# Optimization experiments

Measured on AMD Instinct MI355X. Metric: run time of the kernel, lower is better.

## Reference

```python
import jax, jax.numpy as jnp
import numpy as np
import math

EPS_LN = 1e-5
SCALE = 16.0  # cosine_sim_scale


def layer_norm(x, g):
    mean = jnp.mean(x, axis=-1, keepdims=True)
    var = jnp.var(x, axis=-1, keepdims=True)  # biased, matches unbiased=False
    return (x - mean) * jax.lax.rsqrt(var + EPS_LN) * g


def l2norm(t):
    n = jnp.linalg.norm(t, axis=-1, keepdims=True)
    return t / jnp.maximum(n, 1e-12)


def setup_inputs() -> dict:
    key = jax.random.key(0)
    ks = jax.random.split(key, 4)
    b, n, dim, h, dh = 4, 2048, 1024, 8, 64
    inner = h * dh
    x = jax.random.normal(ks[0], (b, n, dim), dtype=jnp.float32)
    Wq = jax.random.normal(ks[1], (dim, inner), dtype=jnp.float32) * (dim ** -0.5)
    Wkv = jax.random.normal(ks[2], (dim, 2 * dh), dtype=jnp.float32) * (dim ** -0.5)
    Wout = jax.random.normal(ks[3], (inner, dim), dtype=jnp.float32) * (inner ** -0.5)
    norm_g = jnp.ones((dim,), dtype=jnp.float32)
    out_norm_g = jnp.ones((dim,), dtype=jnp.float32)
    return {"x": x, "norm_g": norm_g, "Wq": Wq, "Wkv": Wkv, "Wout": Wout,
            "out_norm_g": out_norm_g}


def reference(x, norm_g, Wq, Wkv, Wout, out_norm_g):
    b, n, dim = x.shape
    h = 8
    dh = Wkv.shape[-1] // 2
    xn = layer_norm(x, norm_g)
    q = xn @ Wq                      # [b, n, h*dh]
    kv = xn @ Wkv                    # [b, n, 2*dh]
    k, v = kv[..., :dh], kv[..., dh:]
    q = q.reshape(b, n, h, dh).transpose(0, 2, 1, 3)  # [b, h, n, dh]
    q = q * SCALE                    # cancelled by l2norm, kept for fidelity
    q = l2norm(q)
    k = l2norm(k)
    rs = math.sqrt(SCALE)
    q = q * rs
    k = k * rs
    sim = jnp.einsum('bhid,bjd->bhij', q, k)          # [b, h, n, n]
    attn = jax.nn.softmax(sim.astype(jnp.float32), axis=-1).astype(sim.dtype)
    out = jnp.einsum('bhij,bjd->bhid', attn, v)       # [b, h, n, dh]
    out = out.transpose(0, 2, 1, 3).reshape(b, n, h * dh)
    out = out @ Wout
    return layer_norm(out, out_norm_g)
```

## Files before the change

kernel.cpp:

```cpp
#include <hip/hip_runtime.h>
#include <hip/hip_bf16.h>

typedef __attribute__((ext_vector_type(8))) short short8;
typedef __attribute__((ext_vector_type(4))) float floatx4;
typedef __attribute__((ext_vector_type(16))) float floatx16;

__device__ __forceinline__ float bf2f(ushort u) {
    return __uint_as_float(((unsigned int)u) << 16);
}
__device__ __forceinline__ ushort f2bf(float f) {
    unsigned int u = __float_as_uint(f);
    unsigned int r = (u + 0x7FFFu + ((u >> 16) & 1u)) >> 16;
    return (ushort)r;
}
__device__ __forceinline__ unsigned int pk2(float a, float b) {
    union { __hip_bfloat162 h; unsigned int u; } cv;
    cv.h = __float22bfloat162_rn(make_float2(a, b));
    return cv.u;
}
__device__ __forceinline__ float scrub(float v, float lim) {
    return fminf(fmaxf(v, -lim), lim);
}
__device__ __forceinline__ void glds16(const ushort* g, ushort* l) {
    __builtin_amdgcn_global_load_lds((const __attribute__((address_space(1))) void*)g,
                                     (__attribute__((address_space(3))) void*)l, 16, 0, 0);
}

__device__ __forceinline__ bool detect_bf16(const ushort* __restrict__ probe) {
    const int lane = threadIdx.x & 63;
    ushort u = probe[(lane & 31) * 2];
    int e = (u >> 7) & 0xFF;
    bool pl = (e >= 117) && (e <= 131) && (lane < 32);
    return __popcll(__ballot(pl)) >= 16;
}

__device__ __forceinline__ void do_transpose(const void* __restrict__ in,
                                             ushort* __restrict__ out,
                                             int bx, int by, int in_rs, int out_rs,
                                             bool ib, ushort* tile ) {
    const int tx = threadIdx.x & 31, ty = threadIdx.x >> 5;
    #pragma unroll
    for (int rr = 0; rr < 32; rr += 8) {
        size_t idx = (size_t)(by * 32 + ty + rr) * in_rs + bx * 32 + tx;
        float v = ib ? bf2f(((const ushort*)in)[idx]) : ((const float*)in)[idx];
        tile[(ty + rr) * 33 + tx] = f2bf(scrub(v, 1e8f));
    }
    __syncthreads();
    #pragma unroll
    for (int rr = 0; rr < 32; rr += 8) {
        int r = bx * 32 + ty + rr;
        int c = by * 32 + tx;
        out[(size_t)r * out_rs + c] = tile[tx * 33 + (ty + rr)];
    }
}

__global__ __launch_bounds__(256) void prep_kernel(const void* __restrict__ xin,
                                                   const void* __restrict__ gin,
                                                   const void* __restrict__ Wq,
                                                   const void* __restrict__ Wkv,
                                                   ushort* __restrict__ xn,
                                                   ushort* __restrict__ wcatT,
                                                   const ushort* __restrict__ probe) {
    const bool ib = detect_bf16(probe);
    const int id = blockIdx.x;
    __shared__ ushort tile[32 * 33];
    __shared__ float red[8];

    if (id >= 8192) {
        if (id < 8704) {
            int t = id - 8192;
            do_transpose(Wq, wcatT, t & 15, t >> 4, 512, 1024, ib, tile);
        } else {
            int t = id - 8704;
            do_transpose(Wkv, wcatT + (size_t)512 * 1024, t & 3, t >> 2, 128, 1024, ib, tile);
        }
        return;
    }

    const int row = id;
    const int tid = threadIdx.x;
    float v0, v1, v2, v3, g0, g1, g2, g3;
    if (ib) {
        uint2 u = *(const uint2*)((const ushort*)xin + (size_t)row * 1024 + tid * 4);
        v0 = bf2f((ushort)(u.x & 0xFFFF)); v1 = bf2f((ushort)(u.x >> 16));
        v2 = bf2f((ushort)(u.y & 0xFFFF)); v3 = bf2f((ushort)(u.y >> 16));
        uint2 gu = *(const uint2*)((const ushort*)gin + tid * 4);
        g0 = bf2f((ushort)(gu.x & 0xFFFF)); g1 = bf2f((ushort)(gu.x >> 16));
        g2 = bf2f((ushort)(gu.y & 0xFFFF)); g3 = bf2f((ushort)(gu.y >> 16));
    } else {
        float4 xv = *(const float4*)((const float*)xin + (size_t)row * 1024 + tid * 4);
        v0 = xv.x; v1 = xv.y; v2 = xv.z; v3 = xv.w;
        float4 gv = *(const float4*)((const float*)gin + tid * 4);
        g0 = gv.x; g1 = gv.y; g2 = gv.z; g3 = gv.w;
    }
    v0 = scrub(v0, 1e8f); v1 = scrub(v1, 1e8f); v2 = scrub(v2, 1e8f); v3 = scrub(v3, 1e8f);
    g0 = scrub(g0, 1e8f); g1 = scrub(g1, 1e8f); g2 = scrub(g2, 1e8f); g3 = scrub(g3, 1e8f);

    float s  = v0 + v1 + v2 + v3;
    float sq = v0 * v0 + v1 * v1 + v2 * v2 + v3 * v3;
    #pragma unroll
    for (int off = 1; off < 64; off <<= 1) {
        s  += __shfl_xor(s, off);
        sq += __shfl_xor(sq, off);
    }
    const int w = tid >> 6, lane = tid & 63;
    if (lane == 0) { red[w] = s; red[w + 4] = sq; }
    __syncthreads();
    float S  = red[0] + red[1] + red[2] + red[3];
    float SQ = red[4] + red[5] + red[6] + red[7];

    float mean = S * (1.0f / 1024.0f);
    float var  = SQ * (1.0f / 1024.0f) - mean * mean;
    float rstd = rsqrtf(fmaxf(var, 0.0f) + 1e-5f);

    uint2 ov;
    ov.x = pk2((v0 - mean) * rstd * g0, (v1 - mean) * rstd * g1);
    ov.y = pk2((v2 - mean) * rstd * g2, (v3 - mean) * rstd * g3);
    *(uint2*)(xn + (size_t)row * 1024 + tid * 4) = ov;
}

__global__ __launch_bounds__(256) void wout_tr_kernel(const void* __restrict__ Wout,
                                                      ushort* __restrict__ woT,
                                                      const ushort* __restrict__ probe) {
    const bool ib = detect_bf16(probe);
    __shared__ ushort tile[32 * 33];
    do_transpose(Wout, woT, blockIdx.x, blockIdx.y, 1024, 512, ib, tile);
}

__global__ __launch_bounds__(256) void ln2_kernel(const ushort* __restrict__ y,
                                                  const void* __restrict__ gin,
                                                  void* __restrict__ out,
                                                  const ushort* __restrict__ probe) {
    const bool ob = detect_bf16(probe);
    const int row = blockIdx.x;
    const int tid = threadIdx.x;

    uint2 u = *(const uint2*)(y + (size_t)row * 1024 + tid * 4);
    float v0 = scrub(bf2f((ushort)(u.x & 0xFFFF)), 1e8f);
    float v1 = scrub(bf2f((ushort)(u.x >> 16)),    1e8f);
    float v2 = scrub(bf2f((ushort)(u.y & 0xFFFF)), 1e8f);
    float v3 = scrub(bf2f((ushort)(u.y >> 16)),    1e8f);

    float g0, g1, g2, g3;
    if (ob) {
        uint2 gu = *(const uint2*)((const ushort*)gin + tid * 4);
        g0 = bf2f((ushort)(gu.x & 0xFFFF)); g1 = bf2f((ushort)(gu.x >> 16));
        g2 = bf2f((ushort)(gu.y & 0xFFFF)); g3 = bf2f((ushort)(gu.y >> 16));
    } else {
        float4 gv = *(const float4*)((const float*)gin + tid * 4);
        g0 = gv.x; g1 = gv.y; g2 = gv.z; g3 = gv.w;
    }
    g0 = scrub(g0, 1e8f); g1 = scrub(g1, 1e8f); g2 = scrub(g2, 1e8f); g3 = scrub(g3, 1e8f);

    float s  = v0 + v1 + v2 + v3;
    float sq = v0 * v0 + v1 * v1 + v2 * v2 + v3 * v3;
    #pragma unroll
    for (int off = 1; off < 64; off <<= 1) {
        s  += __shfl_xor(s, off);
        sq += __shfl_xor(sq, off);
    }
    __shared__ float red[8];
    const int w = tid >> 6, lane = tid & 63;
    if (lane == 0) { red[w] = s; red[w + 4] = sq; }
    __syncthreads();
    float S  = red[0] + red[1] + red[2] + red[3];
    float SQ = red[4] + red[5] + red[6] + red[7];

    float mean = S * (1.0f / 1024.0f);
    float var  = SQ * (1.0f / 1024.0f) - mean * mean;
    float rstd = rsqrtf(fmaxf(var, 0.0f) + 1e-5f);

    float o0 = (v0 - mean) * rstd * g0;
    float o1 = (v1 - mean) * rstd * g1;
    float o2 = (v2 - mean) * rstd * g2;
    float o3 = (v3 - mean) * rstd * g3;
    if (ob) {
        uint2 ov;
        ov.x = pk2(o0, o1);
        ov.y = pk2(o2, o3);
        *(uint2*)((ushort*)out + (size_t)row * 1024 + tid * 4) = ov;
    } else {
        *(float4*)((float*)out + (size_t)row * 1024 + tid * 4) = make_float4(o0, o1, o2, o3);
    }
}

__global__ __launch_bounds__(256) void gemm_qkv(const ushort* __restrict__ A,
                                                const ushort* __restrict__ Bt,
                                                ushort* __restrict__ qb,
                                                ushort* __restrict__ kb,
                                                ushort* __restrict__ vt) {
    __shared__ ushort a_t[64 * 32];
    __shared__ ushort b_t[64 * 32];

    const int bx = blockIdx.x;
    const int n0 = bx * 64, m0 = blockIdx.y * 64;
    const int tid = threadIdx.x;
    const int w = tid >> 6, lane = tid & 63;
    const int fm = lane & 15, quad = lane >> 4;
    const int K = 1024;

    const ushort* ag = A + (size_t)(m0 + (tid >> 2)) * K + (tid & 3) * 8;
    const ushort* bg = Bt + (size_t)(n0 + (tid >> 2)) * K + (tid & 3) * 8;
    ushort* la = a_t + w * 512;
    ushort* lb = b_t + w * 512;

    floatx4 acc[4];
    floatx4 zero4 = {0.0f, 0.0f, 0.0f, 0.0f};
    #pragma unroll
    for (int nt = 0; nt < 4; nt++) acc[nt] = zero4;

    union U8 { uint4 u4; short8 s8; };

    for (int k0 = 0; k0 < K; k0 += 32) {
        __syncthreads();
        glds16(ag + k0, la);
        glds16(bg + k0, lb);
        __syncthreads();

        U8 af;
        af.u4 = *(const uint4*)&a_t[(w * 16 + fm) * 32 + quad * 8];
        #pragma unroll
        for (int nt = 0; nt < 4; nt++) {
            U8 bf;
            bf.u4 = *(const uint4*)&b_t[(nt * 16 + fm) * 32 + quad * 8];
            acc[nt] = __builtin_amdgcn_mfma_f32_16x16x32_bf16(af.s8, bf.s8, acc[nt], 0, 0, 0);
        }
    }

    if (bx < 9) {
        const float qsc = (bx < 8) ? 5.7707801636f : 4.0f;
        float sc[4];
        #pragma unroll
        for (int r = 0; r < 4; r++) {
            float ss = acc[0][r] * acc[0][r] + acc[1][r] * acc[1][r]
                     + acc[2][r] * acc[2][r] + acc[3][r] * acc[3][r];
            ss += __shfl_xor(ss, 1);
            ss += __shfl_xor(ss, 2);
            ss += __shfl_xor(ss, 4);
            ss += __shfl_xor(ss, 8);
            sc[r] = qsc / fmaxf(sqrtf(ss), 1e-12f);
        }
        ushort* op;
        int rs;
        if (bx < 8) { op = qb + n0; rs = 512; }
        else        { op = kb;      rs = 64;  }
        #pragma unroll
        for (int nt = 0; nt < 4; nt++)
            #pragma unroll
            for (int r = 0; r < 4; r++)
                op[(size_t)(m0 + w * 16 + quad * 4 + r) * rs + nt * 16 + fm] =
                    f2bf(acc[nt][r] * sc[r]);
    } else {
        const int b = m0 >> 11;
        const int jb = (m0 & 2047) + w * 16 + quad * 4;
        ushort* vb = vt + (size_t)b * 64 * 2048 + jb;
        #pragma unroll
        for (int nt = 0; nt < 4; nt++) {
            uint2 pv;
            pv.x = pk2(acc[nt][0], acc[nt][1]);
            pv.y = pk2(acc[nt][2], acc[nt][3]);
            *(uint2*)(vb + (size_t)(nt * 16 + fm) * 2048) = pv;
        }
    }
}

__global__ __launch_bounds__(256) void gemm_bt128(const ushort* __restrict__ A,
                                                  const ushort* __restrict__ Bt,
                                                  ushort* __restrict__ C,
                                                  int M, int N, int K) {
    __shared__ ushort a_t[128][32];
    __shared__ ushort b_t[128][32];

    const int n0 = blockIdx.x * 128, m0 = blockIdx.y * 128;
    const int tid = threadIdx.x;
    const int w = tid >> 6, lane = tid & 63;
    const int fm = lane & 15, quad = lane >> 4;

    const int c0 = tid, c1 = tid + 256;
    const ushort* ag0 = A + (size_t)(m0 + (c0 >> 2)) * K + (c0 & 3) * 8;
    const ushort* ag1 = A + (size_t)(m0 + (c1 >> 2)) * K + (c1 & 3) * 8;
    const ushort* bg0 = Bt + (size_t)(n0 + (c0 >> 2)) * K + (c0 & 3) * 8;
    const ushort* bg1 = Bt + (size_t)(n0 + (c1 >> 2)) * K + (c1 & 3) * 8;
    ushort* la0 = &a_t[0][0] + w * 512;
    ushort* la1 = &a_t[0][0] + 2048 + w * 512;
    ushort* lb0 = &b_t[0][0] + w * 512;
    ushort* lb1 = &b_t[0][0] + 2048 + w * 512;

    floatx4 acc[2][8];
    floatx4 zero4 = {0.0f, 0.0f, 0.0f, 0.0f};
    #pragma unroll
    for (int mt = 0; mt < 2; mt++)
        #pragma unroll
        for (int nt = 0; nt < 8; nt++) acc[mt][nt] = zero4;

    union U8 { uint4 u4; short8 s8; };

    for (int k0 = 0; k0 < K; k0 += 32) {
        __syncthreads();
        glds16(ag0 + k0, la0);
        glds16(ag1 + k0, la1);
        glds16(bg0 + k0, lb0);
        glds16(bg1 + k0, lb1);
        __syncthreads();

        U8 af[2];
        #pragma unroll
        for (int mt = 0; mt < 2; mt++)
            af[mt].u4 = *(const uint4*)&a_t[w * 32 + mt * 16 + fm][quad * 8];
        #pragma unroll
        for (int nt = 0; nt < 8; nt++) {
            U8 bf;
            bf.u4 = *(const uint4*)&b_t[nt * 16 + fm][quad * 8];
            acc[0][nt] = __builtin_amdgcn_mfma_f32_16x16x32_bf16(af[0].s8, bf.s8, acc[0][nt], 0, 0, 0);
            acc[1][nt] = __builtin_amdgcn_mfma_f32_16x16x32_bf16(af[1].s8, bf.s8, acc[1][nt], 0, 0, 0);
        }
    }

    #pragma unroll
    for (int mt = 0; mt < 2; mt++)
        #pragma unroll
        for (int nt = 0; nt < 8; nt++)
            #pragma unroll
            for (int r = 0; r < 4; r++)
                C[(size_t)(m0 + w * 32 + mt * 16 + quad * 4 + r) * N + n0 + nt * 16 + fm] =
                    f2bf(acc[mt][nt][r]);
}

__global__ __launch_bounds__(512, 4) void attn_kernel(const ushort* __restrict__ q,
                                                      const ushort* __restrict__ kb,
                                                      const ushort* __restrict__ vt,
                                                      ushort* __restrict__ out) {
    __shared__ ushort k_t[2][2][64 * 64];
    __shared__ ushort v_t[2][2][64 * 64];

    const int i0 = blockIdx.x * 128;
    const int h0 = blockIdx.y, b = blockIdx.z;
    const int tid = threadIdx.x, w = tid >> 6, lane = tid & 63;
    const int qg = w & 3;
    const int kh = w >> 2;
    const int cq = lane & 31;
    const int hi = lane >> 5;
    const int sw = cq & 7;

    union U8 { uint4 u4; short8 s8; };

    const ushort* qbase = q + (size_t)(b * 2048 + i0 + qg * 32 + cq) * 512 + h0 * 64 + hi * 8;
    U8 qf[4];
    #pragma unroll
    for (int dm = 0; dm < 4; dm++) qf[dm].u4 = *(const uint4*)(qbase + dm * 16);

    floatx16 acc0, acc1;
    #pragma unroll
    for (int i = 0; i < 16; i++) { acc0[i] = 0.0f; acc1[i] = 0.0f; }
    float lsum = 0.0f;

    const ushort* kbb = kb + (size_t)b * 2048 * 64;
    const ushort* vtb = vt + (size_t)b * 64 * 2048;

    const int srow = w * 8 + (lane >> 3);
    const int soct = (lane & 7) ^ (srow & 7);
    const int prow = (srow & ~12) | ((srow & 4) << 1) | ((srow & 8) >> 1);
    const ushort* kgl = kbb + (size_t)prow * 64 + soct * 8;
    const ushort* vgl = vtb + (size_t)srow * 2048 + soct * 8;
    ushort* kldb = &k_t[0][0][0] + w * 512;
    ushort* vldb = &v_t[0][0][0] + w * 512;

    int koff[4];
    #pragma unroll
    for (int i = 0; i < 4; i++) koff[i] = ((2 * i + hi) ^ sw) * 8;
    const int rb0 = cq * 64, rb1 = rb0 + 2048;

    auto compute = [&](const ushort* ktile, const ushort* vtile) {
        U8 pb0, pb1, pb2, pb3;
        {
            floatx16 st;
            #pragma unroll
            for (int i = 0; i < 16; i++) st[i] = -23.0831206f;
            #pragma unroll
            for (int dm = 0; dm < 4; dm++) {
                U8 kf;
                kf.u4 = *(const uint4*)&ktile[rb0 + koff[dm]];
                st = __builtin_amdgcn_mfma_f32_32x32x16_bf16(kf.s8, qf[dm].s8, st, 0, 0, 0);
            }
            float p_[16];
            #pragma unroll
            for (int r = 0; r < 16; r++) p_[r] = exp2f(st[r]);
            lsum += (((p_[0] + p_[1]) + (p_[2] + p_[3])) + ((p_[4] + p_[5]) + (p_[6] + p_[7])))
                  + (((p_[8] + p_[9]) + (p_[10] + p_[11])) + ((p_[12] + p_[13]) + (p_[14] + p_[15])));
            pb0.u4.x = pk2(p_[0], p_[1]);   pb0.u4.y = pk2(p_[2], p_[3]);
            pb0.u4.z = pk2(p_[4], p_[5]);   pb0.u4.w = pk2(p_[6], p_[7]);
            pb1.u4.x = pk2(p_[8], p_[9]);   pb1.u4.y = pk2(p_[10], p_[11]);
            pb1.u4.z = pk2(p_[12], p_[13]); pb1.u4.w = pk2(p_[14], p_[15]);
        }
        {
            floatx16 st;
            #pragma unroll
            for (int i = 0; i < 16; i++) st[i] = -23.0831206f;
            #pragma unroll
            for (int dm = 0; dm < 4; dm++) {
                U8 kf;
                kf.u4 = *(const uint4*)&ktile[rb1 + koff[dm]];
                st = __builtin_amdgcn_mfma_f32_32x32x16_bf16(kf.s8, qf[dm].s8, st, 0, 0, 0);
            }
            float p_[16];
            #pragma unroll
            for (int r = 0; r < 16; r++) p_[r] = exp2f(st[r]);
            lsum += (((p_[0] + p_[1]) + (p_[2] + p_[3])) + ((p_[4] + p_[5]) + (p_[6] + p_[7])))
                  + (((p_[8] + p_[9]) + (p_[10] + p_[11])) + ((p_[12] + p_[13]) + (p_[14] + p_[15])));
            pb2.u4.x = pk2(p_[0], p_[1]);   pb2.u4.y = pk2(p_[2], p_[3]);
            pb2.u4.z = pk2(p_[4], p_[5]);   pb2.u4.w = pk2(p_[6], p_[7]);
            pb3.u4.x = pk2(p_[8], p_[9]);   pb3.u4.y = pk2(p_[10], p_[11]);
            pb3.u4.z = pk2(p_[12], p_[13]); pb3.u4.w = pk2(p_[14], p_[15]);
        }
        U8 vf;
        vf.u4 = *(const uint4*)&vtile[rb0 + koff[0]];
        acc0 = __builtin_amdgcn_mfma_f32_32x32x16_bf16(vf.s8, pb0.s8, acc0, 0, 0, 0);
        vf.u4 = *(const uint4*)&vtile[rb0 + koff[1]];
        acc0 = __builtin_amdgcn_mfma_f32_32x32x16_bf16(vf.s8, pb1.s8, acc0, 0, 0, 0);
        vf.u4 = *(const uint4*)&vtile[rb0 + koff[2]];
        acc0 = __builtin_amdgcn_mfma_f32_32x32x16_bf16(vf.s8, pb2.s8, acc0, 0, 0, 0);
        vf.u4 = *(const uint4*)&vtile[rb0 + koff[3]];
        acc0 = __builtin_amdgcn_mfma_f32_32x32x16_bf16(vf.s8, pb3.s8, acc0, 0, 0, 0);
        vf.u4 = *(const uint4*)&vtile[rb1 + koff[0]];
        acc1 = __builtin_amdgcn_mfma_f32_32x32x16_bf16(vf.s8, pb0.s8, acc1, 0, 0, 0);
        vf.u4 = *(const uint4*)&vtile[rb1 + koff[1]];
        acc1 = __builtin_amdgcn_mfma_f32_32x32x16_bf16(vf.s8, pb1.s8, acc1, 0, 0, 0);
        vf.u4 = *(const uint4*)&vtile[rb1 + koff[2]];
        acc1 = __builtin_amdgcn_mfma_f32_32x32x16_bf16(vf.s8, pb2.s8, acc1, 0, 0, 0);
        vf.u4 = *(const uint4*)&vtile[rb1 + koff[3]];
        acc1 = __builtin_amdgcn_mfma_f32_32x32x16_bf16(vf.s8, pb3.s8, acc1, 0, 0, 0);
    };

    glds16(kgl, kldb);
    glds16(kgl + (size_t)1024 * 64, kldb + 4096);
    glds16(vgl, vldb);
    glds16(vgl + 1024, vldb + 4096);
    __syncthreads();

    const ushort* mk = &k_t[0][0][0] + kh * 4096;
    const ushort* mv = &v_t[0][0][0] + kh * 4096;

    for (int s = 0; s < 16; s++) {
        const int cur = (s & 1) << 13;
        const int nxt = cur ^ 8192;
        if (s < 15) {
            const int j = (s + 1) * 64;
            glds16(kgl + (size_t)j * 64, kldb + nxt);
            glds16(kgl + (size_t)(1024 + j) * 64, kldb + nxt + 4096);
            glds16(vgl + j, vldb + nxt);
            glds16(vgl + 1024 + j, vldb + nxt + 4096);
        }
        compute(mk + cur, mv + cur);
        __syncthreads();
    }

    float* xa = (float*)&k_t[0][0][0];
    float* xb = (float*)&v_t[0][0][0];
    if (kh == 1) {
        float* da = xa + (qg * 64 + lane) * 18;
        float* db = xb + (qg * 64 + lane) * 18;
        #pragma unroll
        for (int i = 0; i < 16; i++) { da[i] = acc0[i]; db[i] = acc1[i]; }
        da[16] = lsum;
    }
    __syncthreads();
    if (kh == 1) return;
    {
        const float* sa = xa + (qg * 64 + lane) * 18;
        const float* sb = xb + (qg * 64 + lane) * 18;
        #pragma unroll
        for (int i = 0; i < 16; i++) { acc0[i] += sa[i]; acc1[i] += sb[i]; }
        lsum += sa[16];
    }
    lsum += __shfl_xor(lsum, 32);
    float li = 1.0f / fmaxf(lsum, 1e-30f);

    ushort* ob = out + (size_t)(b * 2048 + i0 + qg * 32 + cq) * 512 + h0 * 64 + hi * 4;
    #pragma unroll
    for (int t = 0; t < 4; t++) {
        uint2 ov;
        ov.x = pk2(acc0[4 * t] * li, acc0[4 * t + 1] * li);
        ov.y = pk2(acc0[4 * t + 2] * li, acc0[4 * t + 3] * li);
        *(uint2*)(ob + t * 8) = ov;
        ov.x = pk2(acc1[4 * t] * li, acc1[4 * t + 1] * li);
        ov.y = pk2(acc1[4 * t + 2] * li, acc1[4 * t + 3] * li);
        *(uint2*)(ob + 32 + t * 8) = ov;
    }
}

extern "C" void kernel_launch(void* const* d_in, const int* in_sizes, int n_in,
                              void* d_out, int out_size, void* d_ws, size_t ws_size,
                              hipStream_t stream) {
    const void* x          = d_in[0];
    const void* norm_g     = d_in[1];
    const void* Wq         = d_in[2];
    const void* Wkv        = d_in[3];
    const void* Wout       = d_in[4];
    const void* out_norm_g = d_in[5];
    const ushort* probe = (const ushort*)d_in[0];
    ushort* ws = (ushort*)d_ws;

    const size_t M1 = 1024 * 1024 / 2;
    ushort* xn    = (ushort*)d_out;
    ushort* ao    = (ushort*)d_out;
    ushort* woT   = (ushort*)((char*)d_out + (8u << 20));
    ushort* qb    = ws;
    ushort* kb    = ws + 8 * M1;
    ushort* vt    = ws + 9 * M1;
    ushort* wcatT = ws + 11 * M1;
    ushort* y     = ws;

    prep_kernel<<<8832, 256, 0, stream>>>(x, norm_g, Wq, Wkv, xn, wcatT, probe);

    gemm_qkv<<<dim3(10, 128), 256, 0, stream>>>(xn, wcatT, qb, kb, vt);

    wout_tr_kernel<<<dim3(32, 16), 256, 0, stream>>>(Wout, woT, probe);

    attn_kernel<<<dim3(16, 8, 4), 512, 0, stream>>>(qb, kb, vt, ao);

    gemm_bt128<<<dim3(8, 64), 256, 0, stream>>>(ao, woT, y, 8192, 1024, 512);

    ln2_kernel<<<8192, 256, 0, stream>>>(y, out_norm_g, d_out, probe);
}
```

Measured before the change: 248.2 us.

## Drop split-K waves in attention; stream full key range per wave

The attention kernel previously ran 512 threads, with two wave groups each handling half of the key sequence and merging partial accumulators through shared memory at the end. It now uses 256 threads, and each wave walks all 32 key tiles of 64 with a smaller double buffer. This removes the LDS reduction and its extra barrier. The P·V MFMAs are interleaved right after each half's exp, which shortens the live ranges of the packed probabilities, and exp2f is replaced by the hardware exp2 builtin. The trade-off is half as many waves per block and twice as many serial iterations and barriers, which may expose more load latency.

```diff
diff --git a/kernel.cpp b/kernel.cpp
--- a/kernel.cpp
+++ b/kernel.cpp
@@ -326,25 +326,23 @@
                     f2bf(acc[mt][nt][r]);
 }
 
-__global__ __launch_bounds__(512, 4) void attn_kernel(const ushort* __restrict__ q,
+__global__ __launch_bounds__(256, 2) void attn_kernel(const ushort* __restrict__ q,
                                                       const ushort* __restrict__ kb,
                                                       const ushort* __restrict__ vt,
                                                       ushort* __restrict__ out) {
-    __shared__ ushort k_t[2][2][64 * 64];
-    __shared__ ushort v_t[2][2][64 * 64];
+    __shared__ ushort k_t[2][64 * 64];
+    __shared__ ushort v_t[2][64 * 64];
 
     const int i0 = blockIdx.x * 128;
     const int h0 = blockIdx.y, b = blockIdx.z;
     const int tid = threadIdx.x, w = tid >> 6, lane = tid & 63;
-    const int qg = w & 3;
-    const int kh = w >> 2;
     const int cq = lane & 31;
     const int hi = lane >> 5;
     const int sw = cq & 7;
 
     union U8 { uint4 u4; short8 s8; };
 
-    const ushort* qbase = q + (size_t)(b * 2048 + i0 + qg * 32 + cq) * 512 + h0 * 64 + hi * 8;
+    const ushort* qbase = q + (size_t)(b * 2048 + i0 + w * 32 + cq) * 512 + h0 * 64 + hi * 8;
     U8 qf[4];
     #pragma unroll
     for (int dm = 0; dm < 4; dm++) qf[dm].u4 = *(const uint4*)(qbase + dm * 16);
@@ -357,22 +355,35 @@
     const ushort* kbb = kb + (size_t)b * 2048 * 64;
     const ushort* vtb = vt + (size_t)b * 64 * 2048;
 
-    const int srow = w * 8 + (lane >> 3);
-    const int soct = (lane & 7) ^ (srow & 7);
-    const int prow = (srow & ~12) | ((srow & 4) << 1) | ((srow & 8) >> 1);
-    const ushort* kgl = kbb + (size_t)prow * 64 + soct * 8;
-    const ushort* vgl = vtb + (size_t)srow * 2048 + soct * 8;
-    ushort* kldb = &k_t[0][0][0] + w * 512;
-    ushort* vldb = &v_t[0][0][0] + w * 512;
+    const int srow0 = w * 16 + (lane >> 3);
+    const int srow1 = srow0 + 8;
+    const int soct = (lane & 7) ^ (srow0 & 7);
+    const int prow0 = (srow0 & ~12) | ((srow0 & 4) << 1) | ((srow0 & 8) >> 1);
+    const int prow1 = (srow1 & ~12) | ((srow1 & 4) << 1) | ((srow1 & 8) >> 1);
+    const ushort* kgl0 = kbb + (size_t)prow0 * 64 + soct * 8;
+    const ushort* kgl1 = kbb + (size_t)prow1 * 64 + soct * 8;
+    const ushort* vgl0 = vtb + (size_t)srow0 * 2048 + soct * 8;
+    const ushort* vgl1 = vtb + (size_t)srow1 * 2048 + soct * 8;
+    ushort* kld = &k_t[0][0] + w * 1024;
+    ushort* vld = &v_t[0][0] + w * 1024;
 
     int koff[4];
     #pragma unroll
     for (int i = 0; i < 4; i++) koff[i] = ((2 * i + hi) ^ sw) * 8;
     const int rb0 = cq * 64, rb1 = rb0 + 2048;
 
+    auto stage = [&](int s, int bufo) {
+        const size_t kj = (size_t)s * 4096;
+        const int vj = s * 64;
+        glds16(kgl0 + kj, kld + bufo);
+        glds16(kgl1 + kj, kld + bufo + 512);
+        glds16(vgl0 + vj, vld + bufo);
+        glds16(vgl1 + vj, vld + bufo + 512);
+    };
+
     auto compute = [&](const ushort* ktile, const ushort* vtile) {
-        U8 pb0, pb1, pb2, pb3;
         {
+            U8 pb0, pb1;
             floatx16 st;
             #pragma unroll
             for (int i = 0; i < 16; i++) st[i] = -23.0831206f;
@@ -384,15 +395,25 @@
             }
             float p_[16];
             #pragma unroll
-            for (int r = 0; r < 16; r++) p_[r] = exp2f(st[r]);
+            for (int r = 0; r < 16; r++) p_[r] = __builtin_amdgcn_exp2f(st[r]);
             lsum += (((p_[0] + p_[1]) + (p_[2] + p_[3])) + ((p_[4] + p_[5]) + (p_[6] + p_[7])))
                   + (((p_[8] + p_[9]) + (p_[10] + p_[11])) + ((p_[12] + p_[13]) + (p_[14] + p_[15])));
             pb0.u4.x = pk2(p_[0], p_[1]);   pb0.u4.y = pk2(p_[2], p_[3]);
             pb0.u4.z = pk2(p_[4], p_[5]);   pb0.u4.w = pk2(p_[6], p_[7]);
             pb1.u4.x = pk2(p_[8], p_[9]);   pb1.u4.y = pk2(p_[10], p_[11]);
             pb1.u4.z = pk2(p_[12], p_[13]); pb1.u4.w = pk2(p_[14], p_[15]);
+            U8 vf;
+            vf.u4 = *(const uint4*)&vtile[rb0 + koff[0]];
+            acc0 = __builtin_amdgcn_mfma_f32_32x32x16_bf16(vf.s8, pb0.s8, acc0, 0, 0, 0);
+            vf.u4 = *(const uint4*)&vtile[rb0 + koff[1]];
+            acc0 = __builtin_amdgcn_mfma_f32_32x32x16_bf16(vf.s8, pb1.s8, acc0, 0, 0, 0);
+            vf.u4 = *(const uint4*)&vtile[rb1 + koff[0]];
+            acc1 = __builtin_amdgcn_mfma_f32_32x32x16_bf16(vf.s8, pb0.s8, acc1, 0, 0, 0);
+            vf.u4 = *(const uint4*)&vtile[rb1 + koff[1]];
+            acc1 = __builtin_amdgcn_mfma_f32_32x32x16_bf16(vf.s8, pb1.s8, acc1, 0, 0, 0);
         }
         {
+            U8 pb2, pb3;
             floatx16 st;
             #pragma unroll
             for (int i = 0; i < 16; i++) st[i] = -23.0831206f;
@@ -404,78 +425,39 @@
             }
             float p_[16];
             #pragma unroll
-            for (int r = 0; r < 16; r++) p_[r] = exp2f(st[r]);
+            for (int r = 0; r < 16; r++) p_[r] = __builtin_amdgcn_exp2f(st[r]);
             lsum += (((p_[0] + p_[1]) + (p_[2] + p_[3])) + ((p_[4] + p_[5]) + (p_[6] + p_[7])))
                   + (((p_[8] + p_[9]) + (p_[10] + p_[11])) + ((p_[12] + p_[13]) + (p_[14] + p_[15])));
             pb2.u4.x = pk2(p_[0], p_[1]);   pb2.u4.y = pk2(p_[2], p_[3]);
             pb2.u4.z = pk2(p_[4], p_[5]);   pb2.u4.w = pk2(p_[6], p_[7]);
             pb3.u4.x = pk2(p_[8], p_[9]);   pb3.u4.y = pk2(p_[10], p_[11]);
             pb3.u4.z = pk2(p_[12], p_[13]); pb3.u4.w = pk2(p_[14], p_[15]);
-        }
-        U8 vf;
-        vf.u4 = *(const uint4*)&vtile[rb0 + koff[0]];
-        acc0 = __builtin_amdgcn_mfma_f32_32x32x16_bf16(vf.s8, pb0.s8, acc0, 0, 0, 0);
-        vf.u4 = *(const uint4*)&vtile[rb0 + koff[1]];
-        acc0 = __builtin_amdgcn_mfma_f32_32x32x16_bf16(vf.s8, pb1.s8, acc0, 0, 0, 0);
-        vf.u4 = *(const uint4*)&vtile[rb0 + koff[2]];
-        acc0 = __builtin_amdgcn_mfma_f32_32x32x16_bf16(vf.s8, pb2.s8, acc0, 0, 0, 0);
-        vf.u4 = *(const uint4*)&vtile[rb0 + koff[3]];
-        acc0 = __builtin_amdgcn_mfma_f32_32x32x16_bf16(vf.s8, pb3.s8, acc0, 0, 0, 0);
-        vf.u4 = *(const uint4*)&vtile[rb1 + koff[0]];
-        acc1 = __builtin_amdgcn_mfma_f32_32x32x16_bf16(vf.s8, pb0.s8, acc1, 0, 0, 0);
-        vf.u4 = *(const uint4*)&vtile[rb1 + koff[1]];
-        acc1 = __builtin_amdgcn_mfma_f32_32x32x16_bf16(vf.s8, pb1.s8, acc1, 0, 0, 0);
-        vf.u4 = *(const uint4*)&vtile[rb1 + koff[2]];
-        acc1 = __builtin_amdgcn_mfma_f32_32x32x16_bf16(vf.s8, pb2.s8, acc1, 0, 0, 0);
-        vf.u4 = *(const uint4*)&vtile[rb1 + koff[3]];
-        acc1 = __builtin_amdgcn_mfma_f32_32x32x16_bf16(vf.s8, pb3.s8, acc1, 0, 0, 0);
+            U8 vf;
+            vf.u4 = *(const uint4*)&vtile[rb0 + koff[2]];
+            acc0 = __builtin_amdgcn_mfma_f32_32x32x16_bf16(vf.s8, pb2.s8, acc0, 0, 0, 0);
+            vf.u4 = *(const uint4*)&vtile[rb0 + koff[3]];
+            acc0 = __builtin_amdgcn_mfma_f32_32x32x16_bf16(vf.s8, pb3.s8, acc0, 0, 0, 0);
+            vf.u4 = *(const uint4*)&vtile[rb1 + koff[2]];
+            acc1 = __builtin_amdgcn_mfma_f32_32x32x16_bf16(vf.s8, pb2.s8, acc1, 0, 0, 0);
+            vf.u4 = *(const uint4*)&vtile[rb1 + koff[3]];
+            acc1 = __builtin_amdgcn_mfma_f32_32x32x16_bf16(vf.s8, pb3.s8, acc1, 0, 0, 0);
+        }
     };
 
-    glds16(kgl, kldb);
-    glds16(kgl + (size_t)1024 * 64, kldb + 4096);
-    glds16(vgl, vldb);
-    glds16(vgl + 1024, vldb + 4096);
+    stage(0, 0);
     __syncthreads();
 
-    const ushort* mk = &k_t[0][0][0] + kh * 4096;
-    const ushort* mv = &v_t[0][0][0] + kh * 4096;
-
-    for (int s = 0; s < 16; s++) {
-        const int cur = (s & 1) << 13;
-        const int nxt = cur ^ 8192;
-        if (s < 15) {
-            const int j = (s + 1) * 64;
-            glds16(kgl + (size_t)j * 64, kldb + nxt);
-            glds16(kgl + (size_t)(1024 + j) * 64, kldb + nxt + 4096);
-            glds16(vgl + j, vldb + nxt);
-            glds16(vgl + 1024 + j, vldb + nxt + 4096);
-        }
-        compute(mk + cur, mv + cur);
+    for (int s = 0; s < 32; s++) {
+        const int cur = (s & 1) << 12;
+        if (s < 31) stage(s + 1, cur ^ 4096);
+        compute(&k_t[0][0] + cur, &v_t[0][0] + cur);
         __syncthreads();
     }
 
-    float* xa = (float*)&k_t[0][0][0];
-    float* xb = (float*)&v_t[0][0][0];
-    if (kh == 1) {
-        float* da = xa + (qg * 64 + lane) * 18;
-        float* db = xb + (qg * 64 + lane) * 18;
-        #pragma unroll
-        for (int i = 0; i < 16; i++) { da[i] = acc0[i]; db[i] = acc1[i]; }
-        da[16] = lsum;
-    }
-    __syncthreads();
-    if (kh == 1) return;
-    {
-        const float* sa = xa + (qg * 64 + lane) * 18;
-        const float* sb = xb + (qg * 64 + lane) * 18;
-        #pragma unroll
-        for (int i = 0; i < 16; i++) { acc0[i] += sa[i]; acc1[i] += sb[i]; }
-        lsum += sa[16];
-    }
     lsum += __shfl_xor(lsum, 32);
     float li = 1.0f / fmaxf(lsum, 1e-30f);
 
-    ushort* ob = out + (size_t)(b * 2048 + i0 + qg * 32 + cq) * 512 + h0 * 64 + hi * 4;
+    ushort* ob = out + (size_t)(b * 2048 + i0 + w * 32 + cq) * 512 + h0 * 64 + hi * 4;
     #pragma unroll
     for (int t = 0; t < 4; t++) {
         uint2 ov;
@@ -516,7 +498,7 @@
 
     wout_tr_kernel<<<dim3(32, 16), 256, 0, stream>>>(Wout, woT, probe);
 
-    attn_kernel<<<dim3(16, 8, 4), 512, 0, stream>>>(qb, kb, vt, ao);
+    attn_kernel<<<dim3(16, 8, 4), 256, 0, stream>>>(qb, kb, vt, ao);
 
     gemm_bt128<<<dim3(8, 64), 256, 0, stream>>>(ao, woT, y, 8192, 1024, 512);
 
```

Measured after the change: 214.1 us. 13.7% less time.
